# Performance work log

Hardware: AMD Instinct MI355X
Metric: run time of the kernel (lower is better)

Reference implementation:

```python
import jax, jax.numpy as jnp
import numpy as np

EPS = 1e-6

def rmsnorm(x, w):
    v = jnp.mean(jnp.square(x), axis=-1, keepdims=True)
    return x * jax.lax.rsqrt(v + EPS) * w

def setup_inputs() -> dict:
    key = jax.random.key(0)
    ks = jax.random.split(key, 12)
    H, Di, L = 2048, 4096, 1024   # hidden, mamba inner (expand*H), seq tokens
    DT, N, K = 128, 16, 4         # dt_rank, d_state, d_conv
    F = 8192                      # MLP intermediate
    s = lambda k, shp, sc: jax.random.normal(k, shp, jnp.float32) * sc
    return dict(
        hidden_states=s(ks[0], (L, H), 1.0),
        in_ln_w=jnp.ones((H,), jnp.float32),
        pre_ff_ln_w=jnp.ones((H,), jnp.float32),
        in_proj_w=s(ks[1], (2 * Di, H), 0.02),
        conv_w=s(ks[2], (Di, K), 0.1),
        conv_b=s(ks[3], (Di,), 0.1),
        x_proj_w=s(ks[4], (DT + 2 * N, Di), 0.02),
        dt_ln_w=jnp.ones((DT,), jnp.float32),
        b_ln_w=jnp.ones((N,), jnp.float32),
        c_ln_w=jnp.ones((N,), jnp.float32),
        dt_proj_w=s(ks[5], (Di, DT), 0.02),
        dt_proj_b=s(ks[6], (Di,), 0.1),
        A=-jnp.exp(jax.random.uniform(ks[7], (Di, N), jnp.float32, -4.0, 0.0)),
        D=jnp.ones((Di,), jnp.float32),
        out_proj_w=s(ks[8], (H, Di), 0.02),
        gate_up_w=s(ks[9], (2 * F, H), 0.02),
        down_w=s(ks[10], (H, F), 0.02),
    )

def reference(hidden_states, in_ln_w, pre_ff_ln_w, in_proj_w, conv_w, conv_b,
              x_proj_w, dt_ln_w, b_ln_w, c_ln_w, dt_proj_w, dt_proj_b,
              A, D, out_proj_w, gate_up_w, down_w):
    residual = hidden_states
    x = rmsnorm(hidden_states, in_ln_w)
    # --- Mamba mixer (prefill / selective_scan path) ---
    proj = x @ in_proj_w.T                          # [L, 2*Di]
    Di = in_proj_w.shape[0] // 2
    h, gate = proj[:, :Di], proj[:, Di:]
    # causal depthwise conv1d, kernel K, left pad K-1, then silu
    K = conv_w.shape[1]
    L = h.shape[0]
    hp = jnp.pad(h, ((K - 1, 0), (0, 0)))           # [L+K-1, Di]
    idx = jnp.arange(L)[:, None] + jnp.arange(K)[None, :]
    h = jnp.einsum('lkd,dk->ld', hp[idx], conv_w) + conv_b
    h = jax.nn.silu(h)
    # ssm parameters
    ssm = h @ x_proj_w.T                            # [L, DT+2N]
    DTr = dt_ln_w.shape[0]
    N = b_ln_w.shape[0]
    dt = rmsnorm(ssm[:, :DTr], dt_ln_w)
    B = rmsnorm(ssm[:, DTr:DTr + N], b_ln_w)
    C = rmsnorm(ssm[:, DTr + N:], c_ln_w)
    delta = jax.nn.softplus(dt @ dt_proj_w.T + dt_proj_b)   # [L, Di]
    # selective scan (discretize then linear recurrence over L)
    dA = jnp.exp(delta[:, :, None] * A[None, :, :])         # [L, Di, N]
    dBu = delta[:, :, None] * B[:, None, :] * h[:, :, None] # [L, Di, N]
    def step(s, inp):
        da, dbu = inp
        s = da * s + dbu
        return s, s
    s0 = jnp.zeros((Di, N), jnp.float32)
    _, states = jax.lax.scan(step, s0, (dA, dBu))           # [L, Di, N]
    y = jnp.einsum('ldn,ln->ld', states, C) + h * D
    y = y * jax.nn.silu(gate)
    mixer_out = y @ out_proj_w.T                    # [L, H]
    # --- residual + pre-FF norm + gated MLP ---
    residual = residual + mixer_out
    x = rmsnorm(residual, pre_ff_ln_w)
    gu = x @ gate_up_w.T                            # [L, 2F]
    F = down_w.shape[1]
    x = jax.nn.silu(gu[:, :F]) * gu[:, F:]
    ff = x @ down_w.T
    return residual + ff
```

## Files before the change

### kernel.cpp

```cpp
#include <hip/hip_runtime.h>
#include <math.h>

typedef unsigned short u16;
typedef __bf16 bf16x8 __attribute__((ext_vector_type(8)));
typedef short s16x8 __attribute__((ext_vector_type(8)));
typedef short s16x4 __attribute__((ext_vector_type(4)));
typedef float f32x4 __attribute__((ext_vector_type(4)));

__device__ __forceinline__ u16 f2bf(float f) {
  union { float f; unsigned u; } v; v.f = f;
  unsigned u = v.u;
  unsigned r = u + 0x7fffu + ((u >> 16) & 1u);
  return (u16)(r >> 16);
}
__device__ __forceinline__ float bf2f(u16 h) {
  union { unsigned u; float f; } v; v.u = ((unsigned)h) << 16;
  return v.f;
}
__device__ __forceinline__ float fast_softplus(float x) {
  return (x > 20.f) ? x : __logf(1.f + __expf(x));
}
__device__ __forceinline__ float fast_sig(float x) {
  return __builtin_amdgcn_rcpf(1.f + __expf(-x));
}

__device__ __forceinline__ void gld_lds16(const u16* g, u16* l) {
  __builtin_amdgcn_global_load_lds(
      (const __attribute__((address_space(1))) unsigned int*)g,
      (__attribute__((address_space(3))) unsigned int*)l, 16, 0, 0);
}

__global__ __launch_bounds__(256)
void f32_to_bf16_k(const float* __restrict__ src, u16* __restrict__ dst,
                   int n, int n_valid) {
  int i = (blockIdx.x * 256 + threadIdx.x) * 4;
  if (i >= n) return;
  s16x4 o;
  if (i + 3 < n_valid) {
    float4 v = *(const float4*)(src + i);
    o[0] = (short)f2bf(v.x); o[1] = (short)f2bf(v.y);
    o[2] = (short)f2bf(v.z); o[3] = (short)f2bf(v.w);
  } else {
    o[0] = 0; o[1] = 0; o[2] = 0; o[3] = 0;
  }
  *(s16x4*)(dst + i) = o;
}

template <int BN, int MODE, int SPLITK>
__global__ __launch_bounds__(256)
void gemm2(const u16* __restrict__ A, const u16* __restrict__ B,
           float* __restrict__ C, u16* __restrict__ Cb,
           const u16* __restrict__ aux, int M, int Nc, int K) {
  constexpr int NJ = BN / 32;
  constexpr int BISS = BN / 32;
  constexpr int ABUF = 64 * 64;
  constexpr int BBUF = BN * 64;
  __shared__ __align__(16) u16 As[2 * ABUF];
  __shared__ __align__(16) u16 Bs[2 * BBUF];
  const int tid = threadIdx.x;
  const int tm0 = blockIdx.y * 64;
  const int tn0 = blockIdx.x * BN;
  const int kslice = K / SPLITK;
  const int k0 = blockIdx.z * kslice;
  const int wave = tid >> 6;
  const int lane = tid & 63;
  const int wm = (wave >> 1) * 32;
  const int wn = (wave & 1) * (BN / 2);
  const int frow = lane & 15;
  const int fc = lane >> 4;
  const int rmask = frow & 7;

  const int r0 = tid >> 3;
  const int csw = (((tid & 7) ^ (r0 & 7)) << 3);
  const u16* gA = A + (size_t)(tm0 + r0) * K + k0 + csw;
  const u16* gB = B + (size_t)(tn0 + r0) * K + k0 + csw;
  u16* lA = &As[tid * 8];
  u16* lB = &Bs[tid * 8];

  f32x4 acc[2][NJ];
  f32x4 zero = {0.f, 0.f, 0.f, 0.f};
#pragma unroll
  for (int i = 0; i < 2; ++i)
#pragma unroll
    for (int j = 0; j < NJ; ++j) acc[i][j] = zero;

  auto stage = [&](int bi) {
    gld_lds16(gA, lA + bi * ABUF);
    gld_lds16(gA + (size_t)32 * K, lA + bi * ABUF + 2048);
#pragma unroll
    for (int b = 0; b < BISS; ++b)
      gld_lds16(gB + (size_t)32 * b * K, lB + bi * BBUF + b * 2048);
    gA += 64; gB += 64;
  };

  stage(0);
  const int nt = kslice >> 6;
  int buf = 0;
  for (int kt = 0; kt < nt; ++kt) {
    const int nb = buf ^ 1;
    if (kt + 1 < nt) {
      stage(nb);
      if constexpr (BN == 64) asm volatile("s_waitcnt vmcnt(4)" ::: "memory");
      else                    asm volatile("s_waitcnt vmcnt(6)" ::: "memory");
    } else {
      asm volatile("s_waitcnt vmcnt(0)" ::: "memory");
    }
    __builtin_amdgcn_s_barrier();
    __builtin_amdgcn_sched_barrier(0);
    const int ao = buf * ABUF, bo = buf * BBUF;
#pragma unroll
    for (int s = 0; s < 2; ++s) {
      bf16x8 af[2], bfr[NJ];
#pragma unroll
      for (int i = 0; i < 2; ++i) {
        int addr = ao + (wm + i * 16 + frow) * 64 + (((s * 4 + fc) ^ rmask) << 3);
        af[i] = __builtin_bit_cast(bf16x8, *(const s16x8*)&As[addr]);
      }
#pragma unroll
      for (int j = 0; j < NJ; ++j) {
        int addr = bo + (wn + j * 16 + frow) * 64 + (((s * 4 + fc) ^ rmask) << 3);
        bfr[j] = __builtin_bit_cast(bf16x8, *(const s16x8*)&Bs[addr]);
      }
#pragma unroll
      for (int i = 0; i < 2; ++i)
#pragma unroll
        for (int j = 0; j < NJ; ++j)
          acc[i][j] = __builtin_amdgcn_mfma_f32_16x16x32_bf16(af[i], bfr[j], acc[i][j], 0, 0, 0);
    }
    __builtin_amdgcn_s_barrier();
    buf = nb;
  }
  const int ccol = lane & 15;
  const int crow = (lane >> 4) * 4;
  float* Cp = C + (size_t)blockIdx.z * ((size_t)M * Nc);
#pragma unroll
  for (int i = 0; i < 2; ++i) {
#pragma unroll
    for (int j = 0; j < NJ; ++j) {
      int gn = tn0 + wn + j * 16 + ccol;
      if (gn < Nc) {
        size_t base = (size_t)(tm0 + wm + i * 16 + crow) * Nc + gn;
#pragma unroll
        for (int r = 0; r < 4; ++r) {
          float c = acc[i][j][r];
          size_t idx = base + (size_t)r * Nc;
          if (MODE == 0) {
            Cp[idx] = c;
          } else if (MODE == 1) {
            Cb[idx] = f2bf(c * fast_sig(c));
          } else {
            Cb[idx] = f2bf(c * bf2f(aux[idx]));
          }
        }
      }
    }
  }
}

template <int MODE, int SPLITK>
__global__ __launch_bounds__(256)
void gemm128(const u16* __restrict__ A, const u16* __restrict__ B,
             float* __restrict__ C, u16* __restrict__ Cb,
             const u16* __restrict__ aux, int M, int Nc, int K) {
  __shared__ __align__(16) u16 As[2 * 128 * 64];
  __shared__ __align__(16) u16 Bs[2 * 128 * 64];
  const int tid = threadIdx.x;
  const int tm0 = blockIdx.y * 128;
  const int tn0 = blockIdx.x * 128;
  const int kslice = K / SPLITK;
  const int k0 = blockIdx.z * kslice;
  const int wave = tid >> 6;
  const int lane = tid & 63;
  const int wm = (wave >> 1) * 64;
  const int wn = (wave & 1) * 64;
  const int frow = lane & 15;
  const int fc = lane >> 4;
  const int rmask = frow & 7;

  const int r0 = tid >> 3;
  const int csw = (((tid & 7) ^ (r0 & 7)) << 3);
  const u16* gA = A + (size_t)(tm0 + r0) * K + k0 + csw;
  const u16* gB = B + (size_t)(tn0 + r0) * K + k0 + csw;
  u16* lA = &As[tid * 8];
  u16* lB = &Bs[tid * 8];

  f32x4 acc[4][4];
  f32x4 zero = {0.f, 0.f, 0.f, 0.f};
#pragma unroll
  for (int i = 0; i < 4; ++i)
#pragma unroll
    for (int j = 0; j < 4; ++j) acc[i][j] = zero;

  auto stage = [&](int bi) {
#pragma unroll
    for (int b = 0; b < 4; ++b) {
      gld_lds16(gA + (size_t)(32 * b) * K, lA + bi * 8192 + b * 2048);
      gld_lds16(gB + (size_t)(32 * b) * K, lB + bi * 8192 + b * 2048);
    }
    gA += 64; gB += 64;
  };

  stage(0);
  const int nt = kslice >> 6;
  int buf = 0;
  for (int kt = 0; kt < nt; ++kt) {
    const int nb = buf ^ 1;
    if (kt + 1 < nt) {
      stage(nb);
      asm volatile("s_waitcnt vmcnt(8)" ::: "memory");
    } else {
      asm volatile("s_waitcnt vmcnt(0)" ::: "memory");
    }
    __builtin_amdgcn_s_barrier();
    __builtin_amdgcn_sched_barrier(0);
    const int boff = buf * 8192;
#pragma unroll
    for (int s = 0; s < 2; ++s) {
      bf16x8 af[4], bfr[4];
#pragma unroll
      for (int i = 0; i < 4; ++i) {
        int addr = boff + (wm + i * 16 + frow) * 64 + (((s * 4 + fc) ^ rmask) << 3);
        af[i] = __builtin_bit_cast(bf16x8, *(const s16x8*)&As[addr]);
      }
#pragma unroll
      for (int j = 0; j < 4; ++j) {
        int addr = boff + (wn + j * 16 + frow) * 64 + (((s * 4 + fc) ^ rmask) << 3);
        bfr[j] = __builtin_bit_cast(bf16x8, *(const s16x8*)&Bs[addr]);
      }
#pragma unroll
      for (int i = 0; i < 4; ++i)
#pragma unroll
        for (int j = 0; j < 4; ++j)
          acc[i][j] = __builtin_amdgcn_mfma_f32_16x16x32_bf16(af[i], bfr[j], acc[i][j], 0, 0, 0);
    }
    __builtin_amdgcn_s_barrier();
    buf = nb;
  }

  const int ccol = lane & 15;
  const int crow = (lane >> 4) * 4;
  float* Cp = C + (size_t)blockIdx.z * ((size_t)M * Nc);
#pragma unroll
  for (int i = 0; i < 4; ++i) {
#pragma unroll
    for (int j = 0; j < 4; ++j) {
      int gn = tn0 + wn + j * 16 + ccol;
      size_t base = (size_t)(tm0 + wm + i * 16 + crow) * Nc + gn;
#pragma unroll
      for (int r = 0; r < 4; ++r) {
        float c = acc[i][j][r];
        size_t idx = base + (size_t)r * Nc;
        if (MODE == 0) {
          Cp[idx] = c;
        } else if (MODE == 1) {
          Cb[idx] = f2bf(c * fast_sig(c));
        } else {
          Cb[idx] = f2bf(c * bf2f(aux[idx]));
        }
      }
    }
  }
}

__device__ inline float block_reduce_sum_256(float v) {
  __shared__ float red[4];
  int lane = threadIdx.x & 63, wave = threadIdx.x >> 6;
#pragma unroll
  for (int m = 32; m > 0; m >>= 1) v += __shfl_xor(v, m, 64);
  if (lane == 0) red[wave] = v;
  __syncthreads();
  return red[0] + red[1] + red[2] + red[3];
}

__global__ __launch_bounds__(256)
void rmsnorm2048_k(const float* __restrict__ x, const float* __restrict__ w,
                   u16* __restrict__ y) {
  const int C = 2048;
  const int row = blockIdx.x;
  const int t = threadIdx.x;
  const float4* xr = (const float4*)(x + (size_t)row * C);
  float4 v0 = xr[t];
  float4 v1 = xr[t + 256];
  float ss = v0.x * v0.x + v0.y * v0.y + v0.z * v0.z + v0.w * v0.w +
             v1.x * v1.x + v1.y * v1.y + v1.z * v1.z + v1.w * v1.w;
  float tot = block_reduce_sum_256(ss);
  float sc = rsqrtf(tot * (1.0f / C) + 1e-6f);
  const float4* wr = (const float4*)w;
  float4 w0 = wr[t], w1 = wr[t + 256];
  u16* yr = y + (size_t)row * C;
  s16x4 o0, o1;
  o0[0] = (short)f2bf(v0.x * sc * w0.x); o0[1] = (short)f2bf(v0.y * sc * w0.y);
  o0[2] = (short)f2bf(v0.z * sc * w0.z); o0[3] = (short)f2bf(v0.w * sc * w0.w);
  o1[0] = (short)f2bf(v1.x * sc * w1.x); o1[1] = (short)f2bf(v1.y * sc * w1.y);
  o1[2] = (short)f2bf(v1.z * sc * w1.z); o1[3] = (short)f2bf(v1.w * sc * w1.w);
  *(s16x4*)(yr + t * 4) = o0;
  *(s16x4*)(yr + 1024 + t * 4) = o1;
}

__global__ __launch_bounds__(256)
void add_rmsnorm4_k(const float* __restrict__ a, const float* __restrict__ p,
                    const float* __restrict__ w, float* __restrict__ resid,
                    u16* __restrict__ y) {
  const int C = 2048;
  const size_t S = (size_t)1024 * 2048;
  const int row = blockIdx.x;
  const int t = threadIdx.x;
  const float4* ar = (const float4*)(a + (size_t)row * C);
  float4 v0 = ar[t], v1 = ar[t + 256];
#pragma unroll
  for (int s = 0; s < 4; ++s) {
    const float4* br = (const float4*)(p + s * S + (size_t)row * C);
    float4 u0 = br[t], u1 = br[t + 256];
    v0.x += u0.x; v0.y += u0.y; v0.z += u0.z; v0.w += u0.w;
    v1.x += u1.x; v1.y += u1.y; v1.z += u1.z; v1.w += u1.w;
  }
  float4* rr = (float4*)(resid + (size_t)row * C);
  rr[t] = v0; rr[t + 256] = v1;
  float ss = v0.x * v0.x + v0.y * v0.y + v0.z * v0.z + v0.w * v0.w +
             v1.x * v1.x + v1.y * v1.y + v1.z * v1.z + v1.w * v1.w;
  float tot = block_reduce_sum_256(ss);
  float sc = rsqrtf(tot * (1.0f / C) + 1e-6f);
  const float4* wr = (const float4*)w;
  float4 w0 = wr[t], w1 = wr[t + 256];
  u16* yr = y + (size_t)row * C;
  s16x4 o0, o1;
  o0[0] = (short)f2bf(v0.x * sc * w0.x); o0[1] = (short)f2bf(v0.y * sc * w0.y);
  o0[2] = (short)f2bf(v0.z * sc * w0.z); o0[3] = (short)f2bf(v0.w * sc * w0.w);
  o1[0] = (short)f2bf(v1.x * sc * w1.x); o1[1] = (short)f2bf(v1.y * sc * w1.y);
  o1[2] = (short)f2bf(v1.z * sc * w1.z); o1[3] = (short)f2bf(v1.w * sc * w1.w);
  *(s16x4*)(yr + t * 4) = o0;
  *(s16x4*)(yr + 1024 + t * 4) = o1;
}

__global__ __launch_bounds__(256)
void conv_silu_k(const float* __restrict__ proj, const float* __restrict__ cw,
                 const float* __restrict__ cb, u16* __restrict__ h) {
  const int Di = 4096, LD = 8192;
  int idx = blockIdx.x * 256 + threadIdx.x;
  int d = idx & (Di - 1);
  int l = idx >> 12;
  float4 w = *(const float4*)(cw + (size_t)d * 4);
  float acc = cb[d];
  int ls0 = l - 3;
  if (ls0 >= 0) acc += proj[(size_t)ls0 * LD + d] * w.x;
  if (ls0 + 1 >= 0) acc += proj[(size_t)(ls0 + 1) * LD + d] * w.y;
  if (ls0 + 2 >= 0) acc += proj[(size_t)(ls0 + 2) * LD + d] * w.z;
  acc += proj[(size_t)l * LD + d] * w.w;
  h[idx] = f2bf(acc * fast_sig(acc));
}

__global__ __launch_bounds__(64)
void ssm_norm_k(const float* __restrict__ ssmp, const float* __restrict__ dtw,
                const float* __restrict__ bw, const float* __restrict__ cw,
                u16* __restrict__ dtn, float* __restrict__ Bn,
                float* __restrict__ Cn) {
  const size_t S = (size_t)1024 * 160;
  int l = blockIdx.x;
  int lane = threadIdx.x;
  float d0 = 0.f, d1 = 0.f, bv = 0.f, cv = 0.f;
#pragma unroll
  for (int s = 0; s < 4; ++s) {
    const float* r = ssmp + s * S + (size_t)l * 160;
    d0 += r[lane];
    d1 += r[lane + 64];
    if (lane < 16) {
      bv += r[128 + lane];
      cv += r[144 + lane];
    }
  }
  float sd = d0 * d0 + d1 * d1;
  float sb = bv * bv;
  float sc = cv * cv;
#pragma unroll
  for (int m = 32; m > 0; m >>= 1) {
    sd += __shfl_xor(sd, m, 64);
    sb += __shfl_xor(sb, m, 64);
    sc += __shfl_xor(sc, m, 64);
  }
  float scd = rsqrtf(sd * (1.f / 128.f) + 1e-6f);
  float scb = rsqrtf(sb * (1.f / 16.f) + 1e-6f);
  float scc = rsqrtf(sc * (1.f / 16.f) + 1e-6f);
  dtn[(size_t)l * 128 + lane] = f2bf(d0 * scd * dtw[lane]);
  dtn[(size_t)l * 128 + lane + 64] = f2bf(d1 * scd * dtw[lane + 64]);
  if (lane < 16) {
    Bn[(size_t)l * 16 + lane] = bv * scb * bw[lane];
    Cn[(size_t)l * 16 + lane] = cv * scc * cw[lane];
  }
}

#define NCH 32
#define CHL 32

__global__ __launch_bounds__(256)
void scan_p1(const float* __restrict__ dpre, const float* __restrict__ dtb,
             const u16* __restrict__ h, const float* __restrict__ Bn,
             const float* __restrict__ Amat,
             float* __restrict__ carryA, float* __restrict__ carryS) {
  const int Di = 4096;
  int chunk = blockIdx.x & (NCH - 1);
  int d = (blockIdx.x >> 5) * 256 + threadIdx.x;
  __shared__ float Bs[CHL * 16];
  for (int i = threadIdx.x; i < CHL * 16; i += 256)
    Bs[i] = Bn[(size_t)chunk * CHL * 16 + i];
  __syncthreads();
  float a[16];
#pragma unroll
  for (int q = 0; q < 4; ++q)
    *(float4*)&a[q * 4] = *(const float4*)(Amat + (size_t)d * 16 + q * 4);
  float bias = dtb[d];
  float s[16];
#pragma unroll
  for (int n = 0; n < 16; ++n) s[n] = 0.f;
  float sumdel = 0.f;
  int l0 = chunk * CHL;
#pragma unroll 4
  for (int j = 0; j < CHL; ++j) {
    int l = l0 + j;
    float del = fast_softplus(dpre[(size_t)l * Di + d] + bias);
    float hv = bf2f(h[(size_t)l * Di + d]);
    sumdel += del;
    float c = del * hv;
#pragma unroll
    for (int n = 0; n < 16; ++n) {
      float dA = __expf(del * a[n]);
      s[n] = dA * s[n] + c * Bs[j * 16 + n];
    }
  }
  size_t base = (size_t)chunk * 65536 + (size_t)d * 16;
#pragma unroll
  for (int n = 0; n < 16; ++n) {
    carryA[base + n] = __expf(sumdel * a[n]);
    carryS[base + n] = s[n];
  }
}

__global__ __launch_bounds__(256)
void scan_p2(const float* __restrict__ carryA, float* __restrict__ carryS) {
  int p = blockIdx.x * 256 + threadIdx.x;
  float cin = 0.f;
#pragma unroll
  for (int c = 0; c < NCH; ++c) {
    float av = carryA[(size_t)c * 65536 + p];
    float sv = carryS[(size_t)c * 65536 + p];
    float nx = av * cin + sv;
    carryS[(size_t)c * 65536 + p] = cin;
    cin = nx;
  }
}

__global__ __launch_bounds__(256)
void scan_p3(const float* __restrict__ dpre, const float* __restrict__ dtb,
             const u16* __restrict__ h, const float* __restrict__ Bn,
             const float* __restrict__ Cn, const float* __restrict__ Amat,
             const float* __restrict__ Dw, const float* __restrict__ proj,
             const float* __restrict__ carryS, u16* __restrict__ y) {
  const int Di = 4096;
  int chunk = blockIdx.x & (NCH - 1);
  int d = (blockIdx.x >> 5) * 256 + threadIdx.x;
  __shared__ float Bs[CHL * 16];
  __shared__ float Cs[CHL * 16];
  for (int i = threadIdx.x; i < CHL * 16; i += 256) {
    Bs[i] = Bn[(size_t)chunk * CHL * 16 + i];
    Cs[i] = Cn[(size_t)chunk * CHL * 16 + i];
  }
  __syncthreads();
  float a[16];
#pragma unroll
  for (int q = 0; q < 4; ++q)
    *(float4*)&a[q * 4] = *(const float4*)(Amat + (size_t)d * 16 + q * 4);
  float bias = dtb[d];
  float Dd = Dw[d];
  float s[16];
  size_t base = (size_t)chunk * 65536 + (size_t)d * 16;
#pragma unroll
  for (int q = 0; q < 4; ++q)
    *(float4*)&s[q * 4] = *(const float4*)(carryS + base + q * 4);
  int l0 = chunk * CHL;
#pragma unroll 2
  for (int j = 0; j < CHL; ++j) {
    int l = l0 + j;
    float del = fast_softplus(dpre[(size_t)l * Di + d] + bias);
    float hv = bf2f(h[(size_t)l * Di + d]);
    float c = del * hv;
    float p = 0.f;
#pragma unroll
    for (int n = 0; n < 16; ++n) {
      float dA = __expf(del * a[n]);
      s[n] = dA * s[n] + c * Bs[j * 16 + n];
      p += s[n] * Cs[j * 16 + n];
    }
    float g = proj[(size_t)l * 8192 + 4096 + d];
    float yv = p + hv * Dd;
    y[(size_t)l * Di + d] = f2bf(yv * g * fast_sig(g));
  }
}

__global__ __launch_bounds__(256)
void add4_k(float* __restrict__ out, const float* __restrict__ p) {
  const size_t S = (size_t)1024 * 2048;
  int i = blockIdx.x * 256 + threadIdx.x;
  float4 a = ((const float4*)out)[i];
#pragma unroll
  for (int s = 0; s < 4; ++s) {
    float4 b = ((const float4*)(p + s * S))[i];
    a.x += b.x; a.y += b.y; a.z += b.z; a.w += b.w;
  }
  ((float4*)out)[i] = a;
}

extern "C" void kernel_launch(void* const* d_in, const int* in_sizes, int n_in,
                              void* d_out, int out_size, void* d_ws, size_t ws_size,
                              hipStream_t stream) {
  const float* hidden      = (const float*)d_in[0];
  const float* in_ln_w     = (const float*)d_in[1];
  const float* pre_ff_ln_w = (const float*)d_in[2];
  const float* in_proj_w   = (const float*)d_in[3];
  const float* conv_w      = (const float*)d_in[4];
  const float* conv_b      = (const float*)d_in[5];
  const float* x_proj_w    = (const float*)d_in[6];
  const float* dt_ln_w     = (const float*)d_in[7];
  const float* b_ln_w      = (const float*)d_in[8];
  const float* c_ln_w      = (const float*)d_in[9];
  const float* dt_proj_w   = (const float*)d_in[10];
  const float* dt_proj_b   = (const float*)d_in[11];
  const float* Amat        = (const float*)d_in[12];
  const float* Dw          = (const float*)d_in[13];
  const float* out_proj_w  = (const float*)d_in[14];
  const float* gate_up_w   = (const float*)d_in[15];
  const float* down_w      = (const float*)d_in[16];
  float* out = (float*)d_out;
  float* ws = (float*)d_ws;

  const int L = 1024, H = 2048, Di = 4096, F = 8192;

  u16*   wbuf   = (u16*)ws;
  float* carryA = ws + 2097152;
  float* carryS = ws + 4194304;
  float* proj   = ws + 8388608;
  float* dpre   = ws + 16777216;
  float* ssmp   = ws + 16777216;
  u16*   hbuf   = (u16*)(ws + 20971520);
  u16*   xnorm  = (u16*)(ws + 23068672);
  u16*   dtn    = (u16*)(ws + 24281088);
  float* Bn     = ws + 24346624;
  float* Cn     = ws + 24363008;
  u16*   ybuf   = (u16*)(ws + 24379392);
  float* mixp   = ws + 8388608;
  u16*   x2     = (u16*)(ws + 18874368);
  u16*   sg     = (u16*)(ws + 8388608);
  u16*   x3     = (u16*)(ws + 12582912);
  float* ffp    = ws + 16777216;

  rmsnorm2048_k<<<L, 256, 0, stream>>>(hidden, in_ln_w, xnorm);
  f32_to_bf16_k<<<16384, 256, 0, stream>>>(in_proj_w, wbuf, 16777216, 16777216);
  gemm128<0, 1><<<dim3(64, 8), 256, 0, stream>>>(xnorm, wbuf, proj, nullptr, nullptr, L, 8192, 2048);
  conv_silu_k<<<(L * Di) / 256, 256, 0, stream>>>(proj, conv_w, conv_b, hbuf);
  f32_to_bf16_k<<<1024, 256, 0, stream>>>(x_proj_w, wbuf, 1048576, 655360);
  gemm2<64, 0, 4><<<dim3(4, 16, 4), 256, 0, stream>>>(hbuf, wbuf, ssmp, nullptr, nullptr, L, 160, 4096);
  ssm_norm_k<<<L, 64, 0, stream>>>(ssmp, dt_ln_w, b_ln_w, c_ln_w, dtn, Bn, Cn);
  f32_to_bf16_k<<<512, 256, 0, stream>>>(dt_proj_w, wbuf, 524288, 524288);
  gemm2<128, 0, 1><<<dim3(32, 16), 256, 0, stream>>>(dtn, wbuf, dpre, nullptr, nullptr, L, 4096, 128);
  scan_p1<<<16 * NCH, 256, 0, stream>>>(dpre, dt_proj_b, hbuf, Bn, Amat, carryA, carryS);
  scan_p2<<<256, 256, 0, stream>>>(carryA, carryS);
  scan_p3<<<16 * NCH, 256, 0, stream>>>(dpre, dt_proj_b, hbuf, Bn, Cn, Amat, Dw, proj, carryS, ybuf);
  f32_to_bf16_k<<<8192, 256, 0, stream>>>(out_proj_w, wbuf, 8388608, 8388608);
  gemm128<0, 4><<<dim3(16, 8, 4), 256, 0, stream>>>(ybuf, wbuf, mixp, nullptr, nullptr, L, 2048, 4096);
  add_rmsnorm4_k<<<L, 256, 0, stream>>>(hidden, mixp, pre_ff_ln_w, out, x2);
  f32_to_bf16_k<<<16384, 256, 0, stream>>>(gate_up_w, wbuf, 16777216, 16777216);
  gemm128<1, 1><<<dim3(64, 8), 256, 0, stream>>>(x2, wbuf, nullptr, sg, nullptr, L, 8192, 2048);
  f32_to_bf16_k<<<16384, 256, 0, stream>>>(gate_up_w + 16777216, wbuf, 16777216, 16777216);
  gemm128<2, 1><<<dim3(64, 8), 256, 0, stream>>>(x2, wbuf, nullptr, x3, sg, L, 8192, 2048);
  f32_to_bf16_k<<<16384, 256, 0, stream>>>(down_w, wbuf, 16777216, 16777216);
  gemm128<0, 4><<<dim3(16, 8, 4), 256, 0, stream>>>(x3, wbuf, ffp, nullptr, nullptr, L, 2048, 8192);
  add4_k<<<(L * H / 4) / 256, 256, 0, stream>>>(out, ffp);
}
```

Before: 636.7 us.

## Fuse fp32-to-bf16 weight conversion into GEMM B-tile loading

The large GEMMs now read fp32 weights straight from global memory into registers, convert them to bf16 with packed convert instructions, and write them into swizzled LDS. This removes five separate conversion kernels that each read fp32 and wrote a bf16 copy of every large weight matrix. In exchange, each GEMM tile loads B at twice the byte width through registers rather than async global-to-LDS. Weight tiles are also reconverted by every M-tile block, which adds VALU and register pressure and an extra LDS wait per iteration.

```diff
diff --git a/kernel.cpp b/kernel.cpp
--- a/kernel.cpp
+++ b/kernel.cpp
@@ -22,6 +22,11 @@
 }
 __device__ __forceinline__ float fast_sig(float x) {
   return __builtin_amdgcn_rcpf(1.f + __expf(-x));
+}
+__device__ __forceinline__ unsigned cvtpk_bf16(float lo, float hi) {
+  unsigned r;
+  asm volatile("v_cvt_pk_bf16_f32 %0, %1, %2" : "=v"(r) : "v"(lo), "v"(hi));
+  return r;
 }
 
 __device__ __forceinline__ void gld_lds16(const u16* g, u16* l) {
@@ -159,11 +164,11 @@
 
 template <int MODE, int SPLITK>
 __global__ __launch_bounds__(256)
-void gemm128(const u16* __restrict__ A, const u16* __restrict__ B,
-             float* __restrict__ C, u16* __restrict__ Cb,
-             const u16* __restrict__ aux, int M, int Nc, int K) {
-  __shared__ __align__(16) u16 As[2 * 128 * 64];
-  __shared__ __align__(16) u16 Bs[2 * 128 * 64];
+void gemm128f(const u16* __restrict__ A, const float* __restrict__ Bw,
+              float* __restrict__ C, u16* __restrict__ Cb,
+              const u16* __restrict__ aux, int M, int Nc, int K) {
+  __shared__ __align__(16) u16 As[2 * 8192];
+  __shared__ __align__(16) u16 Bs[2 * 8192];
   const int tid = threadIdx.x;
   const int tm0 = blockIdx.y * 128;
   const int tn0 = blockIdx.x * 128;
@@ -180,9 +185,9 @@
   const int r0 = tid >> 3;
   const int csw = (((tid & 7) ^ (r0 & 7)) << 3);
   const u16* gA = A + (size_t)(tm0 + r0) * K + k0 + csw;
-  const u16* gB = B + (size_t)(tn0 + r0) * K + k0 + csw;
   u16* lA = &As[tid * 8];
-  u16* lB = &Bs[tid * 8];
+  const float* gBf = Bw + (size_t)(tn0 + r0) * K + k0 + (tid & 7) * 8;
+  u16* lBw = &Bs[r0 * 64 + csw];
 
   f32x4 acc[4][4];
   f32x4 zero = {0.f, 0.f, 0.f, 0.f};
@@ -191,23 +196,47 @@
 #pragma unroll
     for (int j = 0; j < 4; ++j) acc[i][j] = zero;
 
-  auto stage = [&](int bi) {
+  float4 brg[4][2];
+  auto loadB = [&]() {
 #pragma unroll
     for (int b = 0; b < 4; ++b) {
+      const float* p = gBf + (size_t)(32 * b) * K;
+      brg[b][0] = *(const float4*)p;
+      brg[b][1] = *(const float4*)(p + 4);
+    }
+    gBf += 64;
+  };
+  auto stageA = [&](int bi) {
+#pragma unroll
+    for (int b = 0; b < 4; ++b)
       gld_lds16(gA + (size_t)(32 * b) * K, lA + bi * 8192 + b * 2048);
-      gld_lds16(gB + (size_t)(32 * b) * K, lB + bi * 8192 + b * 2048);
-    }
-    gA += 64; gB += 64;
+    gA += 64;
   };
-
-  stage(0);
+  auto writeB = [&](int bi) {
+#pragma unroll
+    for (int b = 0; b < 4; ++b) {
+      uint4 o;
+      o.x = cvtpk_bf16(brg[b][0].x, brg[b][0].y);
+      o.y = cvtpk_bf16(brg[b][0].z, brg[b][0].w);
+      o.z = cvtpk_bf16(brg[b][1].x, brg[b][1].y);
+      o.w = cvtpk_bf16(brg[b][1].z, brg[b][1].w);
+      *(uint4*)(lBw + bi * 8192 + b * 2048) = o;
+    }
+  };
+
+  loadB();
+  stageA(0);
+  writeB(0);
+  asm volatile("s_waitcnt vmcnt(0) lgkmcnt(0)" ::: "memory");
+
   const int nt = kslice >> 6;
   int buf = 0;
   for (int kt = 0; kt < nt; ++kt) {
     const int nb = buf ^ 1;
     if (kt + 1 < nt) {
-      stage(nb);
-      asm volatile("s_waitcnt vmcnt(8)" ::: "memory");
+      loadB();
+      stageA(nb);
+      asm volatile("s_waitcnt vmcnt(12)" ::: "memory");
     } else {
       asm volatile("s_waitcnt vmcnt(0)" ::: "memory");
     }
@@ -232,6 +261,10 @@
 #pragma unroll
         for (int j = 0; j < 4; ++j)
           acc[i][j] = __builtin_amdgcn_mfma_f32_16x16x32_bf16(af[i], bfr[j], acc[i][j], 0, 0, 0);
+    }
+    if (kt + 1 < nt) {
+      writeB(nb);
+      asm volatile("s_waitcnt lgkmcnt(0)" ::: "memory");
     }
     __builtin_amdgcn_s_barrier();
     buf = nb;
@@ -552,8 +585,7 @@
   float* ffp    = ws + 16777216;
 
   rmsnorm2048_k<<<L, 256, 0, stream>>>(hidden, in_ln_w, xnorm);
-  f32_to_bf16_k<<<16384, 256, 0, stream>>>(in_proj_w, wbuf, 16777216, 16777216);
-  gemm128<0, 1><<<dim3(64, 8), 256, 0, stream>>>(xnorm, wbuf, proj, nullptr, nullptr, L, 8192, 2048);
+  gemm128f<0, 1><<<dim3(64, 8), 256, 0, stream>>>(xnorm, in_proj_w, proj, nullptr, nullptr, L, 8192, 2048);
   conv_silu_k<<<(L * Di) / 256, 256, 0, stream>>>(proj, conv_w, conv_b, hbuf);
   f32_to_bf16_k<<<1024, 256, 0, stream>>>(x_proj_w, wbuf, 1048576, 655360);
   gemm2<64, 0, 4><<<dim3(4, 16, 4), 256, 0, stream>>>(hbuf, wbuf, ssmp, nullptr, nullptr, L, 160, 4096);
@@ -563,14 +595,10 @@
   scan_p1<<<16 * NCH, 256, 0, stream>>>(dpre, dt_proj_b, hbuf, Bn, Amat, carryA, carryS);
   scan_p2<<<256, 256, 0, stream>>>(carryA, carryS);
   scan_p3<<<16 * NCH, 256, 0, stream>>>(dpre, dt_proj_b, hbuf, Bn, Cn, Amat, Dw, proj, carryS, ybuf);
-  f32_to_bf16_k<<<8192, 256, 0, stream>>>(out_proj_w, wbuf, 8388608, 8388608);
-  gemm128<0, 4><<<dim3(16, 8, 4), 256, 0, stream>>>(ybuf, wbuf, mixp, nullptr, nullptr, L, 2048, 4096);
+  gemm128f<0, 4><<<dim3(16, 8, 4), 256, 0, stream>>>(ybuf, out_proj_w, mixp, nullptr, nullptr, L, 2048, 4096);
   add_rmsnorm4_k<<<L, 256, 0, stream>>>(hidden, mixp, pre_ff_ln_w, out, x2);
-  f32_to_bf16_k<<<16384, 256, 0, stream>>>(gate_up_w, wbuf, 16777216, 16777216);
-  gemm128<1, 1><<<dim3(64, 8), 256, 0, stream>>>(x2, wbuf, nullptr, sg, nullptr, L, 8192, 2048);
-  f32_to_bf16_k<<<16384, 256, 0, stream>>>(gate_up_w + 16777216, wbuf, 16777216, 16777216);
-  gemm128<2, 1><<<dim3(64, 8), 256, 0, stream>>>(x2, wbuf, nullptr, x3, sg, L, 8192, 2048);
-  f32_to_bf16_k<<<16384, 256, 0, stream>>>(down_w, wbuf, 16777216, 16777216);
-  gemm128<0, 4><<<dim3(16, 8, 4), 256, 0, stream>>>(x3, wbuf, ffp, nullptr, nullptr, L, 2048, 8192);
+  gemm128f<1, 1><<<dim3(64, 8), 256, 0, stream>>>(x2, gate_up_w, nullptr, sg, nullptr, L, 8192, 2048);
+  gemm128f<2, 1><<<dim3(64, 8), 256, 0, stream>>>(x2, gate_up_w + 16777216, nullptr, x3, sg, L, 8192, 2048);
+  gemm128f<0, 4><<<dim3(16, 8, 4), 256, 0, stream>>>(x3, down_w, ffp, nullptr, nullptr, L, 2048, 8192);
   add4_k<<<(L * H / 4) / 256, 256, 0, stream>>>(out, ffp);
 }
```

After: 696.2 us. +9.3%, slower.
